# Kernel tuning notes

Hardware: AMD Instinct MI355X
Metric: run time of the kernel (lower is better)

The kernel has to match this reference:

```python
import jax, jax.numpy as jnp
import numpy as np

LATENT = 256
HIDDEN = 512
MAX_NODES = 64
TAU = 1.0
BATCH = 128
IDX_I, IDX_J = np.triu_indices(MAX_NODES, k=1)  # P = 2016 pairs
EPS = 1e-10


def fixed_positional_encoding(max_len, d_model):
    pos = np.arange(max_len)[:, None].astype(np.float32)
    div = np.exp(np.arange(0, d_model, 2).astype(np.float32) * (-np.log(10000.0) / d_model))
    pe = np.zeros((max_len, d_model), dtype=np.float32)
    pe[:, 0::2] = np.sin(pos * div)
    pe[:, 1::2] = np.cos(pos * div)
    return jnp.asarray(pe)


def setup_inputs() -> dict:
    key = jax.random.key(0)
    ks = jax.random.split(key, 20)

    def unif(k, shape, fan):
        bound = 1.0 / np.sqrt(fan)
        return jax.random.uniform(k, shape, jnp.float32, -bound, bound)

    inp = {}
    inp["z"] = jax.random.normal(ks[0], (BATCH, LATENT), jnp.float32)
    inp["n_nodes"] = jax.random.randint(ks[1], (BATCH,), 1, MAX_NODES + 1)  # lengths >= 1
    inp["n_edges"] = 100
    inp["gumbel_u"] = jax.random.uniform(ks[2], (BATCH, len(IDX_I), 2), jnp.float32)
    # learned params
    inp["emb"] = jax.random.normal(ks[3], (MAX_NODES, LATENT), jnp.float32)
    inp["pe"] = fixed_positional_encoding(MAX_NODES, LATENT)
    inp["W_pre"] = unif(ks[4], (LATENT, 2 * LATENT), 2 * LATENT)
    inp["b_pre"] = unif(ks[5], (LATENT,), 2 * LATENT)
    # GRU layer 0 (input LATENT) and layer 1 (input HIDDEN), torch layout [3H, in]/[3H, H]
    inp["Wih0"] = unif(ks[6], (3 * HIDDEN, LATENT), HIDDEN)
    inp["Whh0"] = unif(ks[7], (3 * HIDDEN, HIDDEN), HIDDEN)
    inp["bih0"] = unif(ks[8], (3 * HIDDEN,), HIDDEN)
    inp["bhh0"] = unif(ks[9], (3 * HIDDEN,), HIDDEN)
    inp["Wih1"] = unif(ks[10], (3 * HIDDEN, HIDDEN), HIDDEN)
    inp["Whh1"] = unif(ks[11], (3 * HIDDEN, HIDDEN), HIDDEN)
    inp["bih1"] = unif(ks[12], (3 * HIDDEN,), HIDDEN)
    inp["bhh1"] = unif(ks[13], (3 * HIDDEN,), HIDDEN)
    inp["node_W"] = unif(ks[14], (HIDDEN, HIDDEN), HIDDEN)
    inp["adj_W1"] = unif(ks[15], (HIDDEN, 2 * HIDDEN), 2 * HIDDEN)
    inp["adj_b1"] = unif(ks[16], (HIDDEN,), 2 * HIDDEN)
    inp["adj_W2"] = unif(ks[17], (2, HIDDEN), HIDDEN)
    inp["adj_b2"] = unif(ks[18], (2,), HIDDEN)
    return inp


def gru_layer(x, Wih, Whh, bih, bhh):
    # x: [B, T, D] -> outputs [B, T, H], torch GRU gate math
    xt = jnp.swapaxes(x, 0, 1)  # [T, B, D]
    gi_all = jnp.einsum("tbd,gd->tbg", xt, Wih) + bih  # precompute input gates
    H = Whh.shape[1]

    def step(h, gi):
        gh = h @ Whh.T + bhh
        ir, iz, inn = gi[:, :H], gi[:, H:2 * H], gi[:, 2 * H:]
        hr, hz, hn = gh[:, :H], gh[:, H:2 * H], gh[:, 2 * H:]
        r = jax.nn.sigmoid(ir + hr)
        zg = jax.nn.sigmoid(iz + hz)
        n = jnp.tanh(inn + r * hn)
        h_new = (1.0 - zg) * n + zg * h
        return h_new, h_new

    h0 = jnp.zeros((x.shape[0], H), x.dtype)
    _, ys = jax.lax.scan(step, h0, gi_all)
    return jnp.swapaxes(ys, 0, 1)  # [B, T, H]


def reference(z, n_nodes, n_edges, gumbel_u, emb, pe, W_pre, b_pre,
              Wih0, Whh0, bih0, bhh0, Wih1, Whh1, bih1, bhh1,
              node_W, adj_W1, adj_b1, adj_W2, adj_b2):
    B = z.shape[0]
    M = MAX_NODES
    # build RNN input: broadcast latent + sinusoidal PE, concat learned pos embedding
    seq = z[:, None, :] + pe[None]                              # [B, M, L]
    pos = jnp.broadcast_to(emb[None], (B, M, LATENT))           # [B, M, L]
    seq = jnp.concatenate([seq, pos], axis=-1)                  # [B, M, 2L]
    seq = seq @ W_pre.T + b_pre                                 # [B, M, L]
    mask = jnp.arange(M)[None, :] < n_nodes[:, None]            # [B, M]
    seq = seq * mask[:, :, None]
    # GRU (packed-sequence semantics == run full padded seq, zero padded outputs)
    h1 = gru_layer(seq, Wih0, Whh0, bih0, bhh0)
    rnn_out = gru_layer(h1, Wih1, Whh1, bih1, bhh1)
    rnn_out = rnn_out * mask[:, :, None]
    node_emb = rnn_out @ node_W.T                               # [B, M, H]
    # gather upper-triangle pairs -> MLP -> 2-way logits
    emb_i = node_emb[:, IDX_I, :]
    emb_j = node_emb[:, IDX_J, :]
    pair = jnp.concatenate([emb_i, emb_j], axis=-1)             # [B, P, 2H]
    hmid = jax.nn.relu(pair @ adj_W1.T + adj_b1)
    logits = hmid @ adj_W2.T + adj_b2                           # [B, P, 2]
    # gumbel-softmax, hard (straight-through)
    g = -jnp.log(-jnp.log(gumbel_u + EPS) + EPS)
    y_soft = jax.nn.softmax((logits + g) / TAU, axis=-1)
    y_hard = jax.nn.one_hot(jnp.argmax(y_soft, axis=-1), 2, dtype=y_soft.dtype)
    y = jax.lax.stop_gradient(y_hard - y_soft) + y_soft
    vals = y[..., 0]                                            # [B, P]
    # scatter into dense symmetric adjacency, mask by valid nodes
    adj = jnp.zeros((B, M, M), z.dtype).at[:, IDX_I, IDX_J].set(vals)
    adj = adj + jnp.swapaxes(adj, 1, 2)
    mask2d = (mask[:, :, None] & mask[:, None, :]).astype(adj.dtype)
    return adj * mask2d
```

## Files before the change

kernel.cpp:

```cpp
#include <hip/hip_runtime.h>
#include <math.h>

#define LATENT 256
#define HIDDEN 512
#define MAXN   64
#define BATCH  128
#define NPAIR  2016
#define G3     1536

#define HT_S   65536
#define GIT_S  196608
#define WT_S   1048576

__global__ __launch_bounds__(256) void pre_kernel(
    const float* __restrict__ z, const float* __restrict__ pe,
    const float* __restrict__ emb, const float* __restrict__ W_pre,
    const float* __restrict__ b_pre, float* __restrict__ ZC,
    float* __restrict__ adj,
    const float* __restrict__ adj_W1, const float* __restrict__ node_W,
    float* __restrict__ WAB,
    const float* __restrict__ Whh0, const float* __restrict__ Wih1,
    const float* __restrict__ Whh1, float* __restrict__ WT)
{
  __shared__ float s1[256];
  __shared__ float s2[256];
  int blk = blockIdx.x;
  int o = threadIdx.x;
  if (blk < 192) {
    int row = blk;
    if (row < 32) {
      int x = row * 256 + o;
      int b = x >> 6, d = x & 63;
      adj[(size_t)b * 4096 + d * 65] = 0.f;
    }
    const float* wr = W_pre + (size_t)o * 512;
    if (row < 128) {
      s1[o] = z[row * 256 + o];
      __syncthreads();
      float acc = 0.f;
      #pragma unroll 8
      for (int k = 0; k < 256; k += 4) {
        float4 w4 = *(const float4*)(wr + k);
        float4 x4 = *(const float4*)(&s1[k]);
        acc += x4.x * w4.x; acc += x4.y * w4.y; acc += x4.z * w4.z; acc += x4.w * w4.w;
      }
      ZC[row * 256 + o] = acc;
    } else {
      int m = row - 128;
      s1[o] = pe[m * 256 + o];
      s2[o] = emb[m * 256 + o];
      __syncthreads();
      float acc = b_pre[o];
      #pragma unroll 8
      for (int k = 0; k < 256; k += 4) {
        float4 w4 = *(const float4*)(wr + k);
        float4 x4 = *(const float4*)(&s1[k]);
        acc += x4.x * w4.x; acc += x4.y * w4.y; acc += x4.z * w4.z; acc += x4.w * w4.w;
      }
      #pragma unroll 8
      for (int k = 0; k < 256; k += 4) {
        float4 w4 = *(const float4*)(wr + 256 + k);
        float4 x4 = *(const float4*)(&s2[k]);
        acc += x4.x * w4.x; acc += x4.y * w4.y; acc += x4.z * w4.z; acc += x4.w * w4.w;
      }
      ZC[row * 256 + o] = acc;
    }
  } else if (blk < 448) {
    int idx = blk - 192;
    int k = (idx & 1) * 256 + o;
    int o0 = ((idx >> 1) & 63) * 8;
    int sel = idx >> 7;
    const float* a1 = adj_W1 + (sel ? 512 : 0);
    float acc[8] = {0.f, 0.f, 0.f, 0.f, 0.f, 0.f, 0.f, 0.f};
    for (int j = 0; j < 512; j++) {
      float w = node_W[(size_t)j * 512 + k];
      #pragma unroll
      for (int oo = 0; oo < 8; oo++)
        acc[oo] += a1[(size_t)(o0 + oo) * 1024 + j] * w;
    }
    #pragma unroll
    for (int oo = 0; oo < 8; oo++)
      WAB[(size_t)(sel * 512 + o0 + oo) * 512 + k] = acc[oo];
  } else {
    int idx2 = blk - 448;
    int mat = idx2 / 96;
    int r0 = (idx2 % 96) * 16;
    const float* Wsrc = (mat == 0) ? Whh0 : (mat == 1) ? Wih1 : Whh1;
    float* Wd = WT + (size_t)mat * WT_S;
    int r = r0 + (o >> 4);
    int oo = r & 511, g = r >> 9;
    int k0 = (o & 15) * 32;
    const float* src = Wsrc + (size_t)r * 512 + k0;
    for (int k = 0; k < 32; k++)
      Wd[((size_t)(k0 + k) * 512 + oo) * 4 + g] = src[k];
  }
}

template<bool MASK>
__global__ __launch_bounds__(256) void gemm_kernel(
    const float* __restrict__ A, int lda,
    const float* __restrict__ W, int ldw,
    const float* __restrict__ bias,
    float* __restrict__ C, int ldc,
    int M, int N, int K,
    const int* __restrict__ n_nodes)
{
  __shared__ float As[16][136];
  __shared__ float Ws[16][136];
  const int tid = threadIdx.x;
  const int tx = tid & 15, ty = tid >> 4;
  const int row0 = blockIdx.y * 128, col0 = blockIdx.x * 128;

  float acc[8][8];
  #pragma unroll
  for (int i = 0; i < 8; i++)
    #pragma unroll
    for (int j = 0; j < 8; j++) acc[i][j] = 0.f;

  for (int k0 = 0; k0 < K; k0 += 16) {
    #pragma unroll
    for (int s = 0; s < 2; s++) {
      int q = tid + 256 * s;
      int r = q >> 2;
      int c4 = (q & 3) << 2;
      int gm = row0 + r;
      float4 v = make_float4(0.f, 0.f, 0.f, 0.f);
      if (gm < M) {
        v = *(const float4*)(A + (size_t)gm * lda + k0 + c4);
        if (MASK) {
          int bb = gm >> 6, tt = gm & 63;
          if (tt >= n_nodes[bb]) v = make_float4(0.f, 0.f, 0.f, 0.f);
        }
      }
      As[c4 + 0][r] = v.x; As[c4 + 1][r] = v.y; As[c4 + 2][r] = v.z; As[c4 + 3][r] = v.w;
      int gn = col0 + r;
      float4 w = *(const float4*)(W + (size_t)gn * ldw + k0 + c4);
      Ws[c4 + 0][r] = w.x; Ws[c4 + 1][r] = w.y; Ws[c4 + 2][r] = w.z; Ws[c4 + 3][r] = w.w;
    }
    __syncthreads();
    #pragma unroll
    for (int kk = 0; kk < 16; kk++) {
      float4 a0 = *(const float4*)&As[kk][ty * 8];
      float4 a1 = *(const float4*)&As[kk][ty * 8 + 4];
      float4 b0 = *(const float4*)&Ws[kk][tx * 8];
      float4 b1 = *(const float4*)&Ws[kk][tx * 8 + 4];
      float av[8] = {a0.x, a0.y, a0.z, a0.w, a1.x, a1.y, a1.z, a1.w};
      float bv[8] = {b0.x, b0.y, b0.z, b0.w, b1.x, b1.y, b1.z, b1.w};
      #pragma unroll
      for (int i = 0; i < 8; i++)
        #pragma unroll
        for (int j = 0; j < 8; j++)
          acc[i][j] += av[i] * bv[j];
    }
    __syncthreads();
  }

  float bb[8];
  #pragma unroll
  for (int j = 0; j < 8; j++) bb[j] = bias ? bias[col0 + tx * 8 + j] : 0.f;
  #pragma unroll
  for (int i = 0; i < 8; i++) {
    int gm = row0 + ty * 8 + i;
    if (gm < M) {
      float* out = C + (size_t)gm * ldc + col0 + tx * 8;
      float4 o0 = make_float4(acc[i][0] + bb[0], acc[i][1] + bb[1], acc[i][2] + bb[2], acc[i][3] + bb[3]);
      float4 o1 = make_float4(acc[i][4] + bb[4], acc[i][5] + bb[5], acc[i][6] + bb[6], acc[i][7] + bb[7]);
      *(float4*)out = o0;
      *(float4*)(out + 4) = o1;
    }
  }
}

__global__ __launch_bounds__(512) void gru_v5_kernel(
    const float* __restrict__ WT,
    const float* __restrict__ ZCW,
    const float* __restrict__ bih0, const float* __restrict__ bhh0,
    const float* __restrict__ bih1, const float* __restrict__ bhh1,
    const int* __restrict__ n_nodes,
    float* __restrict__ Ht1, float* __restrict__ GIt,
    float* __restrict__ H2t, float* __restrict__ H2row,
    int s)
{
  __shared__ float p_s[8][3][8][32];
  const int tid = threadIdx.x;
  const int plane = blockIdx.y;
  const int o0 = (blockIdx.x >> 2) * 8;
  const int b0 = (blockIdx.x & 3) * 32;

  int t; const float* Wmat; const float* Hin; bool dd;
  if (plane == 0)      { t = s;     Wmat = WT;            Hin = Ht1 + ((t - 1) & 1) * HT_S; dd = (t > 0); }
  else if (plane == 1) { t = s - 1; Wmat = WT + WT_S;     Hin = Ht1 + (t & 1) * HT_S;       dd = true; }
  else                 { t = s - 2; Wmat = WT + 2 * WT_S; Hin = H2t + ((t - 1) & 1) * HT_S; dd = (t > 0); }
  if (t < 0 || t > 63) return;

  float acc[3][4] = {{0.f, 0.f, 0.f, 0.f}, {0.f, 0.f, 0.f, 0.f}, {0.f, 0.f, 0.f, 0.f}};
  const int w = tid >> 6, l = tid & 63;
  const int bg = l & 7, rg = l >> 3;

  if (dd) {
    const float* hp_ = Hin + b0 + bg * 4 + (size_t)(w << 6) * 128;
    const float* wp_ = Wmat + (size_t)(o0 + rg) * 4 + (size_t)(w << 6) * 2048;
    #pragma unroll 4
    for (int k = 0; k < 64; k++) {
      float4 h4 = *(const float4*)(hp_ + (size_t)k * 128);
      float4 w4 = *(const float4*)(wp_ + (size_t)k * 2048);
      acc[0][0] += h4.x * w4.x; acc[0][1] += h4.y * w4.x; acc[0][2] += h4.z * w4.x; acc[0][3] += h4.w * w4.x;
      acc[1][0] += h4.x * w4.y; acc[1][1] += h4.y * w4.y; acc[1][2] += h4.z * w4.y; acc[1][3] += h4.w * w4.y;
      acc[2][0] += h4.x * w4.z; acc[2][1] += h4.y * w4.z; acc[2][2] += h4.z * w4.z; acc[2][3] += h4.w * w4.z;
    }
  }

  *(float4*)&p_s[w][0][rg][bg * 4] = make_float4(acc[0][0], acc[0][1], acc[0][2], acc[0][3]);
  *(float4*)&p_s[w][1][rg][bg * 4] = make_float4(acc[1][0], acc[1][1], acc[1][2], acc[1][3]);
  *(float4*)&p_s[w][2][rg][bg * 4] = make_float4(acc[2][0], acc[2][1], acc[2][2], acc[2][3]);
  __syncthreads();

  if (tid < 256) {
    int b = tid & 31, oi = tid >> 5;
    float s0 = 0.f, s1 = 0.f, s2 = 0.f;
    #pragma unroll
    for (int ww = 0; ww < 8; ww++) {
      s0 += p_s[ww][0][oi][b];
      s1 += p_s[ww][1][oi][b];
      s2 += p_s[ww][2][oi][b];
    }
    const int B = b0 + b, O = o0 + oi;

    if (plane == 0) {
      bool mk = t < n_nodes[B];
      float zr = mk ? ZCW[(size_t)B * G3 + O]        + ZCW[(size_t)(128 + t) * G3 + O]        : 0.f;
      float zz = mk ? ZCW[(size_t)B * G3 + 512 + O]  + ZCW[(size_t)(128 + t) * G3 + 512 + O]  : 0.f;
      float zn = mk ? ZCW[(size_t)B * G3 + 1024 + O] + ZCW[(size_t)(128 + t) * G3 + 1024 + O] : 0.f;
      float ir = zr + bih0[O], iz = zz + bih0[512 + O], inn = zn + bih0[1024 + O];
      float hr = s0 + bhh0[O], hz = s1 + bhh0[512 + O], hn = s2 + bhh0[1024 + O];
      float rg_ = 1.f / (1.f + expf(-(ir + hr)));
      float zg  = 1.f / (1.f + expf(-(iz + hz)));
      float ng  = tanhf(inn + rg_ * hn);
      float hp = (t > 0) ? Ht1[((t - 1) & 1) * HT_S + O * 128 + B] : 0.f;
      Ht1[(t & 1) * HT_S + O * 128 + B] = (1.f - zg) * ng + zg * hp;
    } else if (plane == 1) {
      size_t gb = (size_t)(t & 1) * GIT_S;
      GIt[gb + (size_t)O * 128 + B]          = s0 + bih1[O];
      GIt[gb + (size_t)(512 + O) * 128 + B]  = s1 + bih1[512 + O];
      GIt[gb + (size_t)(1024 + O) * 128 + B] = s2 + bih1[1024 + O];
    } else {
      size_t gb = (size_t)(t & 1) * GIT_S;
      float ir  = GIt[gb + (size_t)O * 128 + B];
      float iz  = GIt[gb + (size_t)(512 + O) * 128 + B];
      float inn = GIt[gb + (size_t)(1024 + O) * 128 + B];
      float hr = s0 + bhh1[O], hz = s1 + bhh1[512 + O], hn = s2 + bhh1[1024 + O];
      float rg_ = 1.f / (1.f + expf(-(ir + hr)));
      float zg  = 1.f / (1.f + expf(-(iz + hz)));
      float ng  = tanhf(inn + rg_ * hn);
      float hp = (t > 0) ? H2t[((t - 1) & 1) * HT_S + O * 128 + B] : 0.f;
      float hnew = (1.f - zg) * ng + zg * hp;
      H2t[(t & 1) * HT_S + O * 128 + B] = hnew;
      H2row[((size_t)(B * 64 + t)) * 512 + O] = hnew;
    }
  }
}

__global__ __launch_bounds__(256) void pair_kernel(
    const float* __restrict__ AB, const float* __restrict__ b1,
    const float* __restrict__ W2, const float* __restrict__ b2,
    const float* __restrict__ gu, const int* __restrict__ n_nodes,
    float* __restrict__ adj)
{
  int wid = blockIdx.x * 4 + (threadIdx.x >> 6);
  int lane = threadIdx.x & 63;
  int b = wid / NPAIR;
  int p = wid - b * NPAIR;

  float fp = (float)p;
  int i = (int)((127.0f - sqrtf(16129.0f - 8.0f * fp)) * 0.5f);
  if (i < 0) i = 0;
  if (i > 62) i = 62;
  while (i < 62 && (i + 1) * (126 - i) / 2 <= p) i++;
  while (i > 0 && i * (127 - i) / 2 > p) i--;
  int j = p - i * (127 - i) / 2 + i + 1;

  const float* arow = AB + ((size_t)(b * 64 + i)) * 1024;
  const float* brow = AB + ((size_t)(b * 64 + j)) * 1024 + 512;
  int k0 = lane * 8;

  float4 a0 = *(const float4*)(arow + k0);
  float4 a1 = *(const float4*)(arow + k0 + 4);
  float4 q0 = *(const float4*)(brow + k0);
  float4 q1 = *(const float4*)(brow + k0 + 4);
  float4 c0 = *(const float4*)(b1 + k0);
  float4 c1 = *(const float4*)(b1 + k0 + 4);

  float h0 = fmaxf(a0.x + q0.x + c0.x, 0.f);
  float h1 = fmaxf(a0.y + q0.y + c0.y, 0.f);
  float h2 = fmaxf(a0.z + q0.z + c0.z, 0.f);
  float h3 = fmaxf(a0.w + q0.w + c0.w, 0.f);
  float h4 = fmaxf(a1.x + q1.x + c1.x, 0.f);
  float h5 = fmaxf(a1.y + q1.y + c1.y, 0.f);
  float h6 = fmaxf(a1.z + q1.z + c1.z, 0.f);
  float h7 = fmaxf(a1.w + q1.w + c1.w, 0.f);

  float4 w00 = *(const float4*)(W2 + k0);
  float4 w01 = *(const float4*)(W2 + k0 + 4);
  float4 w10 = *(const float4*)(W2 + 512 + k0);
  float4 w11 = *(const float4*)(W2 + 512 + k0 + 4);

  float acc0 = h0 * w00.x + h1 * w00.y + h2 * w00.z + h3 * w00.w
             + h4 * w01.x + h5 * w01.y + h6 * w01.z + h7 * w01.w;
  float acc1 = h0 * w10.x + h1 * w10.y + h2 * w10.z + h3 * w10.w
             + h4 * w11.x + h5 * w11.y + h6 * w11.z + h7 * w11.w;

  #pragma unroll
  for (int off = 32; off > 0; off >>= 1) {
    acc0 += __shfl_xor(acc0, off, 64);
    acc1 += __shfl_xor(acc1, off, 64);
  }

  if (lane == 0) {
    float s0 = acc0 + b2[0];
    float s1 = acc1 + b2[1];
    const float* u = gu + ((size_t)(b * NPAIR + p)) * 2;
    float g0 = -logf(-logf(u[0] + 1e-10f) + 1e-10f);
    float g1 = -logf(-logf(u[1] + 1e-10f) + 1e-10f);
    int n = n_nodes[b];
    float val = 0.f;
    if (i < n && j < n) val = ((s0 + g0) >= (s1 + g1)) ? 1.f : 0.f;
    adj[(size_t)b * 4096 + i * 64 + j] = val;
    adj[(size_t)b * 4096 + j * 64 + i] = val;
  }
}

extern "C" void kernel_launch(void* const* d_in, const int* in_sizes, int n_in,
                              void* d_out, int out_size, void* d_ws, size_t ws_size,
                              hipStream_t stream)
{
  (void)in_sizes; (void)n_in; (void)out_size; (void)ws_size;

  const float* z       = (const float*)d_in[0];
  const int*   n_nodes = (const int*)d_in[1];
  const float* gu      = (const float*)d_in[3];
  const float* emb     = (const float*)d_in[4];
  const float* pe      = (const float*)d_in[5];
  const float* W_pre   = (const float*)d_in[6];
  const float* b_pre   = (const float*)d_in[7];
  const float* Wih0    = (const float*)d_in[8];
  const float* Whh0    = (const float*)d_in[9];
  const float* bih0    = (const float*)d_in[10];
  const float* bhh0    = (const float*)d_in[11];
  const float* Wih1    = (const float*)d_in[12];
  const float* Whh1    = (const float*)d_in[13];
  const float* bih1    = (const float*)d_in[14];
  const float* bhh1    = (const float*)d_in[15];
  const float* node_W  = (const float*)d_in[16];
  const float* adj_W1  = (const float*)d_in[17];
  const float* adj_b1  = (const float*)d_in[18];
  const float* adj_W2  = (const float*)d_in[19];
  const float* adj_b2  = (const float*)d_in[20];
  float* adj = (float*)d_out;

  char* ws = (char*)d_ws;
  float* ZC    = (float*)(ws + 0);
  float* ZCW   = (float*)(ws + 196608);
  float* WAB   = (float*)(ws + 1376256);
  float* WT    = (float*)(ws + 3473408);
  float* Ht1   = (float*)(ws + 16056320);
  float* H2t   = (float*)(ws + 16580608);
  float* GIt   = (float*)(ws + 17104896);
  float* H2row = (float*)(ws + 18677760);
  float* AB    = (float*)(ws + 35454976);

  pre_kernel<<<736, 256, 0, stream>>>(z, pe, emb, W_pre, b_pre, ZC, adj,
                                      adj_W1, node_W, WAB,
                                      Whh0, Wih1, Whh1, WT);

  gemm_kernel<false><<<dim3(12, 2), 256, 0, stream>>>(
      ZC, 256, Wih0, 256, nullptr, ZCW, 1536, 192, 1536, 256, nullptr);

  for (int s = 0; s <= 65; s++)
    gru_v5_kernel<<<dim3(256, 3), 512, 0, stream>>>(
        WT, ZCW, bih0, bhh0, bih1, bhh1, n_nodes,
        Ht1, GIt, H2t, H2row, s);

  gemm_kernel<true><<<dim3(8, 64), 256, 0, stream>>>(
      H2row, 512, WAB, 512, nullptr, AB, 1024, 8192, 1024, 512, n_nodes);

  pair_kernel<<<64512, 256, 0, stream>>>(AB, adj_b1, adj_W2, adj_b2, gu, n_nodes, adj);
}
```

Before: 2.028 ms.

## Prefetch GEMM tiles into registers, reorder block mapping, skip masked pairs

The GEMM kernel now loads the next K-tile from global memory into registers while the current tile is being computed, which hides load latency behind the FMA loop. Its grid is transposed so that neighbouring blocks walk along rows, and the GRU kernel's block index is remapped so consecutive blocks cover different output rows for the same batch slice. The pair kernel now exits early for pairs outside the valid node count and writes zeros there, skipping the MLP loads and the Gumbel logs for padded nodes. The changes add register pressure in the GEMM and alter the cache access pattern, and the GRU recurrence (66 launches) probably remains the dominant cost.

```diff
diff --git a/kernel.cpp b/kernel.cpp
--- a/kernel.cpp
+++ b/kernel.cpp
@@ -109,7 +109,7 @@
   __shared__ float Ws[16][136];
   const int tid = threadIdx.x;
   const int tx = tid & 15, ty = tid >> 4;
-  const int row0 = blockIdx.y * 128, col0 = blockIdx.x * 128;
+  const int row0 = blockIdx.x * 128, col0 = blockIdx.y * 128;
 
   float acc[8][8];
   #pragma unroll
@@ -117,7 +117,8 @@
     #pragma unroll
     for (int j = 0; j < 8; j++) acc[i][j] = 0.f;
 
-  for (int k0 = 0; k0 < K; k0 += 16) {
+  float4 va[2], vw[2];
+  auto load_tile = [&](int k0) {
     #pragma unroll
     for (int s = 0; s < 2; s++) {
       int q = tid + 256 * s;
@@ -132,12 +133,24 @@
           if (tt >= n_nodes[bb]) v = make_float4(0.f, 0.f, 0.f, 0.f);
         }
       }
-      As[c4 + 0][r] = v.x; As[c4 + 1][r] = v.y; As[c4 + 2][r] = v.z; As[c4 + 3][r] = v.w;
+      va[s] = v;
       int gn = col0 + r;
-      float4 w = *(const float4*)(W + (size_t)gn * ldw + k0 + c4);
-      Ws[c4 + 0][r] = w.x; Ws[c4 + 1][r] = w.y; Ws[c4 + 2][r] = w.z; Ws[c4 + 3][r] = w.w;
-    }
+      vw[s] = *(const float4*)(W + (size_t)gn * ldw + k0 + c4);
+    }
+  };
+
+  load_tile(0);
+  for (int k0 = 0; k0 < K; k0 += 16) {
     __syncthreads();
+    #pragma unroll
+    for (int s = 0; s < 2; s++) {
+      int q = tid + 256 * s;
+      int r = q >> 2, c4 = (q & 3) << 2;
+      As[c4 + 0][r] = va[s].x; As[c4 + 1][r] = va[s].y; As[c4 + 2][r] = va[s].z; As[c4 + 3][r] = va[s].w;
+      Ws[c4 + 0][r] = vw[s].x; Ws[c4 + 1][r] = vw[s].y; Ws[c4 + 2][r] = vw[s].z; Ws[c4 + 3][r] = vw[s].w;
+    }
+    __syncthreads();
+    if (k0 + 16 < K) load_tile(k0 + 16);
     #pragma unroll
     for (int kk = 0; kk < 16; kk++) {
       float4 a0 = *(const float4*)&As[kk][ty * 8];
@@ -152,7 +165,6 @@
         for (int j = 0; j < 8; j++)
           acc[i][j] += av[i] * bv[j];
     }
-    __syncthreads();
   }
 
   float bb[8];
@@ -184,8 +196,8 @@
   __shared__ float p_s[8][3][8][32];
   const int tid = threadIdx.x;
   const int plane = blockIdx.y;
-  const int o0 = (blockIdx.x >> 2) * 8;
-  const int b0 = (blockIdx.x & 3) * 32;
+  const int o0 = (blockIdx.x & 63) << 3;
+  const int b0 = (blockIdx.x >> 6) << 5;
 
   int t; const float* Wmat; const float* Hin; bool dd;
   if (plane == 0)      { t = s;     Wmat = WT;            Hin = Ht1 + ((t - 1) & 1) * HT_S; dd = (t > 0); }
@@ -279,6 +291,15 @@
   while (i > 0 && i * (127 - i) / 2 > p) i--;
   int j = p - i * (127 - i) / 2 + i + 1;
 
+  int n = n_nodes[b];
+  if (i >= n || j >= n) {
+    if (lane == 0) {
+      adj[(size_t)b * 4096 + i * 64 + j] = 0.f;
+      adj[(size_t)b * 4096 + j * 64 + i] = 0.f;
+    }
+    return;
+  }
+
   const float* arow = AB + ((size_t)(b * 64 + i)) * 1024;
   const float* brow = AB + ((size_t)(b * 64 + j)) * 1024 + 512;
   int k0 = lane * 8;
@@ -321,9 +342,7 @@
     const float* u = gu + ((size_t)(b * NPAIR + p)) * 2;
     float g0 = -logf(-logf(u[0] + 1e-10f) + 1e-10f);
     float g1 = -logf(-logf(u[1] + 1e-10f) + 1e-10f);
-    int n = n_nodes[b];
-    float val = 0.f;
-    if (i < n && j < n) val = ((s0 + g0) >= (s1 + g1)) ? 1.f : 0.f;
+    float val = ((s0 + g0) >= (s1 + g1)) ? 1.f : 0.f;
     adj[(size_t)b * 4096 + i * 64 + j] = val;
     adj[(size_t)b * 4096 + j * 64 + i] = val;
   }
@@ -372,7 +391,7 @@
                                       adj_W1, node_W, WAB,
                                       Whh0, Wih1, Whh1, WT);
 
-  gemm_kernel<false><<<dim3(12, 2), 256, 0, stream>>>(
+  gemm_kernel<false><<<dim3(2, 12), 256, 0, stream>>>(
       ZC, 256, Wih0, 256, nullptr, ZCW, 1536, 192, 1536, 256, nullptr);
 
   for (int s = 0; s <= 65; s++)
@@ -380,7 +399,7 @@
         WT, ZCW, bih0, bhh0, bih1, bhh1, n_nodes,
         Ht1, GIt, H2t, H2row, s);
 
-  gemm_kernel<true><<<dim3(8, 64), 256, 0, stream>>>(
+  gemm_kernel<true><<<dim3(64, 8), 256, 0, stream>>>(
       H2row, 512, WAB, 512, nullptr, AB, 1024, 8192, 1024, 512, n_nodes);
 
   pair_kernel<<<64512, 256, 0, stream>>>(AB, adj_b1, adj_W2, adj_b2, gu, n_nodes, adj);
```

After: 1.947 ms, median of 2. -4.0%, faster.
